# Kernel tuning notes

Hardware: AMD Instinct MI355X
Metric: run time of the kernel (lower is better)

Reference implementation:

```python
import jax, jax.numpy as jnp
import numpy as np


def setup_inputs() -> dict:
    key = jax.random.key(0)
    generated_images = jax.random.normal(key, (64, 3, 256, 256), dtype=jnp.float32)
    return {"generated_images": generated_images}


def reference(generated_images):
    # Original: sum_{i<j} mse(x_i, x_j), mse = mean over per-image elements.
    # Vectorized via Gram matrix: mean((xi-xj)^2) = (|xi|^2 + |xj|^2 - 2 xi.xj)/D
    B = generated_images.shape[0]
    x = generated_images.reshape(B, -1)          # [B, D]
    D = x.shape[1]
    sq = jnp.sum(x * x, axis=-1)                 # [B]
    G = x @ x.T                                  # [B, B]
    pair = sq[:, None] + sq[None, :] - 2.0 * G   # [B, B], squared L2 distances
    # sum over i<j = (sum of all entries - trace)/2; trace is exactly 0
    sum_pairs = jnp.sum(pair) * 0.5 / D
    return -sum_pairs / (B * (B - 1))
```

## Files before the change

kernel.cpp:

```cpp
#include <hip/hip_runtime.h>
#include <hip/hip_bf16.h>


__global__ __launch_bounds__(64) void div_zero_ws(float* __restrict__ acc) {
    acc[0] = 0.0f;
}

__global__ __launch_bounds__(64) void div_main(const float4* __restrict__ x4,
                                               float* __restrict__ acc,
                                               int D4, int B) {
    const int c = blockIdx.x * 64 + threadIdx.x;
    const float4* p = x4 + c;

    float sx = 0.f, sy = 0.f, sz = 0.f, sw = 0.f;
    float sq = 0.f;

    #pragma unroll
    for (int r = 0; r < 64; ++r) {
        float4 v = p[(size_t)r * (size_t)D4];
        sx += v.x; sy += v.y; sz += v.z; sw += v.w;
        sq = fmaf(v.x, v.x, sq);
        sq = fmaf(v.y, v.y, sq);
        sq = fmaf(v.z, v.z, sq);
        sq = fmaf(v.w, v.w, sq);
    }

    float contrib = sx * sx + sy * sy + sz * sz + sw * sw - (float)B * sq;

    #pragma unroll
    for (int off = 32; off > 0; off >>= 1)
        contrib += __shfl_down(contrib, off, 64);

    if (threadIdx.x == 0)
        atomicAdd(acc, contrib);
}

__global__ __launch_bounds__(64) void div_finalize(const float* __restrict__ acc,
                                                   float* __restrict__ out,
                                                   float scale) {
    out[0] = acc[0] * scale;
}

extern "C" void kernel_launch(void* const* d_in, const int* in_sizes, int n_in,
                              void* d_out, int out_size, void* d_ws, size_t ws_size,
                              hipStream_t stream) {
    const float* x = (const float*)d_in[0];
    float* out = (float*)d_out;
    float* acc = (float*)d_ws;

    const int B = 64;
    const int total = in_sizes[0];
    const int D = total / B;
    const int D4 = D / 4;
    const int grid = D4 / 64;

    const float scale = (float)(1.0 / ((double)D * (double)B * (double)(B - 1)));

    div_zero_ws<<<1, 64, 0, stream>>>(acc);
    div_main<<<grid, 64, 0, stream>>>((const float4*)x, acc, D4, B);
    div_finalize<<<1, 64, 0, stream>>>(acc, out, scale);
}
```

Baseline: 90.17 us.

## Split row sums across four wavefronts and replace atomics with two-stage reduction

Each block now uses 256 threads, with four wavefronts each summing 16 of the 64 images for the same 64 columns, and their column sums are combined through shared memory. Each block writes a per-block partial into the workspace instead of doing a global atomicAdd, and a 256-thread finalize kernel reduces the 768 partials. This drops the zero-init kernel launch and atomic contention and gives each thread a shorter dependent load chain. The exchange is extra shared-memory traffic and block barriers, plus a hardcoded grid of 768 blocks that relies on the fixed input size.

```diff
diff --git a/kernel.cpp b/kernel.cpp
--- a/kernel.cpp
+++ b/kernel.cpp
@@ -2,21 +2,22 @@
 #include <hip/hip_bf16.h>
 
 
-__global__ __launch_bounds__(64) void div_zero_ws(float* __restrict__ acc) {
-    acc[0] = 0.0f;
-}
+#define NBLK 768
 
-__global__ __launch_bounds__(64) void div_main(const float4* __restrict__ x4,
-                                               float* __restrict__ acc,
-                                               int D4, int B) {
-    const int c = blockIdx.x * 64 + threadIdx.x;
-    const float4* p = x4 + c;
+__global__ __launch_bounds__(256) void div_main(const float4* __restrict__ x4,
+                                                float* __restrict__ partial,
+                                                int D4) {
+    const int lane = threadIdx.x & 63;
+    const int rg   = threadIdx.x >> 6;
+    const int col  = blockIdx.x * 64 + lane;
+
+    const float4* p = x4 + (size_t)rg * 16 * (size_t)D4 + col;
 
     float sx = 0.f, sy = 0.f, sz = 0.f, sw = 0.f;
     float sq = 0.f;
 
     #pragma unroll
-    for (int r = 0; r < 64; ++r) {
+    for (int r = 0; r < 16; ++r) {
         float4 v = p[(size_t)r * (size_t)D4];
         sx += v.x; sy += v.y; sz += v.z; sw += v.w;
         sq = fmaf(v.x, v.x, sq);
@@ -25,20 +26,46 @@
         sq = fmaf(v.w, v.w, sq);
     }
 
-    float contrib = sx * sx + sy * sy + sz * sz + sw * sw - (float)B * sq;
+    float contrib = -64.0f * sq;
+
+    __shared__ float4 part[3][64];
+    if (rg > 0) part[rg - 1][lane] = make_float4(sx, sy, sz, sw);
+    __syncthreads();
+    if (rg == 0) {
+        #pragma unroll
+        for (int g = 0; g < 3; ++g) {
+            float4 t = part[g][lane];
+            sx += t.x; sy += t.y; sz += t.z; sw += t.w;
+        }
+        contrib += sx * sx + sy * sy + sz * sz + sw * sw;
+    }
 
     #pragma unroll
     for (int off = 32; off > 0; off >>= 1)
         contrib += __shfl_down(contrib, off, 64);
 
+    __shared__ float wsum[4];
+    if (lane == 0) wsum[rg] = contrib;
+    __syncthreads();
     if (threadIdx.x == 0)
-        atomicAdd(acc, contrib);
+        partial[blockIdx.x] = wsum[0] + wsum[1] + wsum[2] + wsum[3];
 }
 
-__global__ __launch_bounds__(64) void div_finalize(const float* __restrict__ acc,
-                                                   float* __restrict__ out,
-                                                   float scale) {
-    out[0] = acc[0] * scale;
+__global__ __launch_bounds__(256) void div_finalize(const float* __restrict__ partial,
+                                                    float* __restrict__ out,
+                                                    float scale) {
+    const int t = threadIdx.x;
+    float v = partial[t] + partial[t + 256] + partial[t + 512];
+
+    #pragma unroll
+    for (int off = 32; off > 0; off >>= 1)
+        v += __shfl_down(v, off, 64);
+
+    __shared__ float wsum[4];
+    if ((t & 63) == 0) wsum[t >> 6] = v;
+    __syncthreads();
+    if (t == 0)
+        out[0] = (wsum[0] + wsum[1] + wsum[2] + wsum[3]) * scale;
 }
 
 extern "C" void kernel_launch(void* const* d_in, const int* in_sizes, int n_in,
@@ -46,17 +73,15 @@
                               hipStream_t stream) {
     const float* x = (const float*)d_in[0];
     float* out = (float*)d_out;
-    float* acc = (float*)d_ws;
+    float* partial = (float*)d_ws;
 
     const int B = 64;
     const int total = in_sizes[0];
     const int D = total / B;
     const int D4 = D / 4;
-    const int grid = D4 / 64;
 
     const float scale = (float)(1.0 / ((double)D * (double)B * (double)(B - 1)));
 
-    div_zero_ws<<<1, 64, 0, stream>>>(acc);
-    div_main<<<grid, 64, 0, stream>>>((const float4*)x, acc, D4, B);
-    div_finalize<<<1, 64, 0, stream>>>(acc, out, scale);
+    div_main<<<NBLK, 256, 0, stream>>>((const float4*)x, partial, D4);
+    div_finalize<<<1, 256, 0, stream>>>(partial, out, scale);
 }
```

After: 80.43 us. -10.8%, faster.
